# Optimization experiments

Measured on AMD Instinct MI355X. Metric: run time of the kernel, lower is better.

The kernel has to match this reference:

```python
import jax, jax.numpy as jnp
from jax import lax
import numpy as np

B, L, DIM = 4, 4096, 512
H, HD = 8, 64            # num_heads, head_dim
CHUNK = 128              # chunk size for chunk-recurrent lightning attention
LN_EPS = 1e-5


def _slopes(h):
    # _build_slope_tensor for power-of-2 heads: 2^(-8*(i+1)/h), cast through fp16
    s = np.array([2.0 ** (-8.0 * (i + 1) / h) for i in range(h)], dtype=np.float32)
    return jnp.asarray(s.astype(np.float16).astype(np.float32))  # [h]


def _layernorm(x, w, b):
    mu = jnp.mean(x, axis=-1, keepdims=True)
    var = jnp.mean((x - mu) ** 2, axis=-1, keepdims=True)
    return (x - mu) * lax.rsqrt(var + LN_EPS) * w + b


def _rmsnorm(x, gamma):
    # F.normalize(x, dim=-1) * sqrt(d) * gamma ; gamma [h,1,d] broadcasts over [b,h,l,d]
    n = x / jnp.maximum(jnp.linalg.norm(x, axis=-1, keepdims=True), 1e-12)
    return n * (HD ** 0.5) * gamma


def _lightning_attn(q, k, v, slopes):
    # q,k,v: [b,h,L,d]; causal linear attention with per-head decay exp(-s*(t-j))
    b, h, l, d = q.shape
    nc = l // CHUNK
    s = slopes[:, None, None]                      # [h,1,1]
    r = jnp.arange(CHUNK, dtype=q.dtype)
    diff = r[:, None] - r[None, :]                 # [C,C]
    Dintra = jnp.where(diff >= 0, jnp.exp(-s * diff), 0.0)   # [h,C,C]
    q_dec = jnp.exp(-slopes[:, None] * r[None, :])           # [h,C] decay from chunk start
    k_dec = jnp.exp(-slopes[:, None] * (CHUNK - r[None, :])) # [h,C] decay to next chunk start
    c_dec = jnp.exp(-slopes * CHUNK)                         # [h]

    def to_chunks(t):
        return t.reshape(b, h, nc, CHUNK, d).transpose(2, 0, 1, 3, 4)  # [nc,b,h,C,d]

    qc, kc, vc = to_chunks(q), to_chunks(k), to_chunks(v)

    def step(kv, inp):
        qi, ki, vi = inp                                       # [b,h,C,d]
        scores = jnp.einsum('bhid,bhjd->bhij', qi, ki) * Dintra[None]
        intra = jnp.einsum('bhij,bhjd->bhid', scores, vi)
        inter = jnp.einsum('bhcd,bhde->bhce', qi * q_dec[None, :, :, None], kv)
        kv = kv * c_dec[None, :, None, None] + jnp.einsum(
            'bhcd,bhce->bhde', ki * k_dec[None, :, :, None], vi)
        return kv, intra + inter

    kv0 = jnp.zeros((b, h, d, d), q.dtype)
    _, out = lax.scan(step, kv0, (qc, kc, vc))                 # [nc,b,h,C,d]
    return out.transpose(1, 2, 0, 3, 4).reshape(b, h, l, d)


def setup_inputs() -> dict:
    key = jax.random.key(0)
    ks = jax.random.split(key, 8)
    std = lambda fan_in: 1.0 / np.sqrt(fan_in)
    return {
        'x': jax.random.normal(ks[0], (B, L, DIM), jnp.float32),
        'ln1_w': jnp.ones((DIM,), jnp.float32),
        'ln1_b': jnp.zeros((DIM,), jnp.float32),
        'rel_bias': 0.02 * jax.random.normal(ks[1], (1, L, DIM), jnp.float32),
        'qkv_w': std(DIM) * jax.random.normal(ks[2], (3 * DIM, DIM), jnp.float32),
        'qkv_b': jnp.zeros((3 * DIM,), jnp.float32),
        'gq': jnp.ones((H, 1, HD), jnp.float32) / (HD ** 0.5),
        'gk': jnp.ones((H, 1, HD), jnp.float32) / (HD ** 0.5),
        'proj_w': std(DIM) * jax.random.normal(ks[3], (DIM, DIM), jnp.float32),
        'proj_b': jnp.zeros((DIM,), jnp.float32),
        'ln2_w': jnp.ones((DIM,), jnp.float32),
        'ln2_b': jnp.zeros((DIM,), jnp.float32),
        'fc1_w': std(DIM) * jax.random.normal(ks[4], (4 * DIM, DIM), jnp.float32),
        'fc1_b': jnp.zeros((4 * DIM,), jnp.float32),
        'fc2_w': std(4 * DIM) * jax.random.normal(ks[5], (DIM, 4 * DIM), jnp.float32),
        'fc2_b': jnp.zeros((DIM,), jnp.float32),
    }


def reference(x, ln1_w, ln1_b, rel_bias, qkv_w, qkv_b, gq, gk,
              proj_w, proj_b, ln2_w, ln2_b, fc1_w, fc1_b, fc2_w, fc2_b):
    slopes = _slopes(H)
    b, l, c = x.shape
    shortcut = x
    h = _layernorm(x, ln1_w, ln1_b)
    # --- LightningAttention ---
    h = h + rel_bias
    qkv = (h @ qkv_w.T + qkv_b).reshape(b, l, 3, H, HD).transpose(2, 0, 3, 1, 4)
    q, k, v = qkv[0], qkv[1], qkv[2]                     # [b,h,l,d]
    q = _rmsnorm(q * (HD ** -0.5), gq)
    k = _rmsnorm(k, gk)
    o = _lightning_attn(q, k, v, slopes)                 # [b,h,l,d]
    o = o.reshape(b, l, c)                               # faithful to source: reshape, no head transpose
    o = o @ proj_w.T + proj_b
    x = o + shortcut
    # --- MLP ---
    shortcut = x
    h = _layernorm(x, ln2_w, ln2_b)
    h = jax.nn.gelu(h @ fc1_w.T + fc1_b, approximate=False)
    h = h @ fc2_w.T + fc2_b
    return h + shortcut
```

## Files before the change

### kernel.cpp

```cpp
#include <hip/hip_runtime.h>
#include <math.h>

typedef unsigned short u16;
typedef __bf16 bf16x8 __attribute__((ext_vector_type(8)));
typedef float f32x4 __attribute__((ext_vector_type(4)));

#define DEVI static __device__ __forceinline__

DEVI float b2f(u16 u) { union { unsigned int i; float f; } w; w.i = ((unsigned int)u) << 16; return w.f; }
DEVI u16 f2b(float f) {
  union { float f; unsigned int i; } w; w.f = f;
  unsigned int r = (w.i + 0x7FFFu + ((w.i >> 16) & 1u)) >> 16;
  return (u16)r;
}
DEVI u16 cvt_bf16(float f) { __bf16 h = (__bf16)f; union { __bf16 h; u16 u; } w; w.h = h; return w.u; }

DEVI float fast_gelu(float v) {
  float x2 = v * v;
  float p = fmaf(0.10294357f, x2, 2.30215855f);
  float ex = exp2f(-v * p);
  return v * __builtin_amdgcn_rcpf(1.0f + ex);
}

__global__ void conv4_kernel(const float* __restrict__ s0, u16* __restrict__ d0, int n0,
                             const float* __restrict__ s1, u16* __restrict__ d1, int n1,
                             const float* __restrict__ s2, u16* __restrict__ d2, int n2,
                             const float* __restrict__ s3, u16* __restrict__ d3, int n3) {
  int i = blockIdx.x * 256 + threadIdx.x;
  int st = gridDim.x * 256;
  int tot = n0 + n1 + n2 + n3;
  for (; i < tot; i += st) {
    int j = i;
    if (j < n0) { d0[j] = f2b(s0[j]); continue; }
    j -= n0;
    if (j < n1) { d1[j] = f2b(s1[j]); continue; }
    j -= n1;
    if (j < n2) { d2[j] = f2b(s2[j]); continue; }
    j -= n2;
    d3[j] = f2b(s3[j]);
  }
}

template<int ADD_REL>
__global__ __launch_bounds__(256) void ln_kernel(
    const float* __restrict__ x, const float* __restrict__ w, const float* __restrict__ bb,
    const float* __restrict__ rel, u16* __restrict__ out) {
  int row = blockIdx.x;
  int t = threadIdx.x;
  const float* xr = x + (size_t)row * 512;
  float v0 = xr[t], v1 = xr[t + 256];
  float s = v0 + v1, ss = v0 * v0 + v1 * v1;
#pragma unroll
  for (int o = 32; o > 0; o >>= 1) { s += __shfl_down(s, o); ss += __shfl_down(ss, o); }
  __shared__ float rs[4], rss[4];
  int lane = t & 63, wid = t >> 6;
  if (lane == 0) { rs[wid] = s; rss[wid] = ss; }
  __syncthreads();
  s = rs[0] + rs[1] + rs[2] + rs[3];
  ss = rss[0] + rss[1] + rss[2] + rss[3];
  float mu = s * (1.0f / 512.0f);
  float inv = rsqrtf(ss * (1.0f / 512.0f) - mu * mu + 1e-5f);
  float o0 = (v0 - mu) * inv * w[t] + bb[t];
  float o1 = (v1 - mu) * inv * w[t + 256] + bb[t + 256];
  if (ADD_REL) {
    const float* rr = rel + (size_t)(row & 4095) * 512;
    o0 += rr[t]; o1 += rr[t + 256];
  }
  u16* orow = out + (size_t)row * 512;
  orow[t] = f2b(o0);
  orow[t + 256] = f2b(o1);
}

template<int EPI, int TM, int NSLOT>
__global__ __launch_bounds__(256) void gemm_bt_kernel(
    const u16* __restrict__ A, const u16* __restrict__ W,
    const float* __restrict__ bias, int M, int N, int K, int NBN,
    const float* __restrict__ resid, u16* __restrict__ outb,
    u16* __restrict__ q_out, u16* __restrict__ k_out, u16* __restrict__ v_out,
    float* __restrict__ outf, const float* __restrict__ gq, const float* __restrict__ gk) {
  constexpr int WM   = TM / 2;
  constexpr int NI   = TM / 32;
  constexpr int CA   = TM / 64;
  constexpr int SLOT = (TM + 128) * 32;
  __shared__ __align__(16) u16 sbuf[NSLOT * SLOT];
  int nwg = gridDim.x, wg = blockIdx.x;
  int wgs = (wg & 7) * (nwg >> 3) + (wg >> 3);
  int bn = wgs % NBN, bm = wgs / NBN;
  int m0 = bm * TM, n0 = bn * 128;
  int t = threadIdx.x, lane = t & 63, wid = t >> 6;
  int wrM = (wid >> 1) * WM, wc = (wid & 1) * 64;
  int fr = lane & 15, fk = (lane >> 4) * 8;
  int srowA = wid * (TM / 4) + (lane >> 2);
  int srowB = wid * 32 + (lane >> 2);
  int scol = (lane & 3) * 8;
  const u16* gA = A + (size_t)(m0 + srowA) * K + scol;
  const u16* gB = W + (size_t)(n0 + srowB) * K + scol;
  f32x4 acc[NI][4] = {};
  auto AS = [&](int sel) { return &sbuf[sel * SLOT]; };
  auto BS = [&](int sel) { return &sbuf[sel * SLOT + TM * 32]; };
  auto STAGE = [&](int sel, int k0) {
    u16* lA = AS(sel) + wid * (CA * 512);
    u16* lB = BS(sel) + wid * 1024;
#pragma unroll
    for (int c = 0; c < CA; ++c)
      __builtin_amdgcn_global_load_lds(gA + k0 + c * 16 * K, lA + c * 512, 16, 0, 0);
    __builtin_amdgcn_global_load_lds(gB + k0,          lB,       16, 0, 0);
    __builtin_amdgcn_global_load_lds(gB + k0 + 16 * K, lB + 512, 16, 0, 0);
  };
  auto COMPUTE = [&](int sel) {
    bf16x8 af[NI], bfr[4];
#pragma unroll
    for (int i = 0; i < NI; ++i) af[i] = *(const bf16x8*)&AS(sel)[(wrM + i * 16 + fr) * 32 + fk];
#pragma unroll
    for (int j = 0; j < 4; ++j) bfr[j] = *(const bf16x8*)&BS(sel)[(wc + j * 16 + fr) * 32 + fk];
#pragma unroll
    for (int i = 0; i < NI; ++i)
#pragma unroll
      for (int j = 0; j < 4; ++j)
        acc[i][j] = __builtin_amdgcn_mfma_f32_16x16x32_bf16(af[i], bfr[j], acc[i][j], 0, 0, 0);
  };
  if constexpr (NSLOT == 2) {
    STAGE(0, 0);
    asm volatile("s_waitcnt vmcnt(0)" ::: "memory");
    __builtin_amdgcn_s_barrier();
    int cur = 0;
    for (int k0 = 0; k0 < K; k0 += 32) {
      if (k0 + 32 < K) STAGE(cur ^ 1, k0 + 32);
      COMPUTE(cur);
      asm volatile("s_waitcnt vmcnt(0)" ::: "memory");
      __builtin_amdgcn_s_barrier();
      cur ^= 1;
    }
  } else {
    STAGE(0, 0);
    STAGE(1, 32);
    int cur = 0, nxt = 2;
    for (int k0 = 0; k0 < K; k0 += 32) {
      if (k0 + 32 < K) {
        if constexpr (CA == 4) { asm volatile("s_waitcnt vmcnt(6)" ::: "memory"); }
        else                   { asm volatile("s_waitcnt vmcnt(4)" ::: "memory"); }
      } else {
        asm volatile("s_waitcnt vmcnt(0)" ::: "memory");
      }
      __builtin_amdgcn_s_barrier();
      if (k0 + 64 < K) {
        STAGE(nxt, k0 + 64);
        nxt = (nxt == 2) ? 0 : nxt + 1;
      }
      COMPUTE(cur);
      cur = (cur == 2) ? 0 : cur + 1;
    }
  }
  __syncthreads();
  int fq = lane >> 4;
  constexpr int LP = 68;
  float* lbuf = (float*)sbuf + wid * 2048;
  float bv[4];
#pragma unroll
  for (int j = 0; j < 4; ++j) bv[j] = bias[n0 + wc + j * 16 + fr];
  int rr = lane >> 2, c0 = (lane & 3) * 16;
  int nb = n0 + wc;
  int which = nb >> 9, head = (nb >> 6) & 7;
  float ggv[16];
  if (EPI == 0 && which != 2) {
    const float* gg = (which == 0) ? gq : gk;
#pragma unroll
    for (int e = 0; e < 16; ++e) ggv[e] = gg[head * 64 + c0 + e];
  }
#pragma unroll
  for (int i = 0; i < NI; ++i) {
#pragma unroll
    for (int j = 0; j < 4; ++j)
#pragma unroll
      for (int jj = 0; jj < 4; ++jj)
        lbuf[(fq * 4 + jj) * LP + j * 16 + fr] = acc[i][j][jj] + bv[j];
    float v[16];
#pragma unroll
    for (int g = 0; g < 4; ++g) {
      f32x4 r4 = *(const f32x4*)&lbuf[rr * LP + c0 + g * 4];
#pragma unroll
      for (int e = 0; e < 4; ++e) v[g * 4 + e] = r4[e];
    }
    int gm = m0 + wrM + i * 16 + rr;
    if (EPI == 0) {
      u16* dst = (which == 0) ? q_out : (which == 1) ? k_out : v_out;
      int b = gm >> 12, l = gm & 4095;
      size_t rowbase = (((size_t)(b * 8 + head) * 4096) + l) * 64 + c0;
      union { u16 h[16]; uint4 q[2]; } pk;
      if (which == 2) {
#pragma unroll
        for (int e = 0; e < 16; ++e) pk.h[e] = cvt_bf16(v[e]);
      } else {
        float ssum = 0.f;
#pragma unroll
        for (int e = 0; e < 16; ++e) ssum += v[e] * v[e];
        ssum += __shfl_xor(ssum, 1);
        ssum += __shfl_xor(ssum, 2);
        float inv = 8.0f / fmaxf(sqrtf(ssum), 1e-12f);
#pragma unroll
        for (int e = 0; e < 16; ++e) pk.h[e] = cvt_bf16(v[e] * inv * ggv[e]);
      }
      *(uint4*)&dst[rowbase] = pk.q[0];
      *(uint4*)&dst[rowbase + 8] = pk.q[1];
    } else if (EPI == 1) {
      size_t idx = (size_t)gm * 512 + n0 + wc + c0;
#pragma unroll
      for (int g = 0; g < 4; ++g) {
        f32x4 r = *(const f32x4*)&resid[idx + g * 4];
        f32x4 o;
#pragma unroll
        for (int e = 0; e < 4; ++e) o[e] = v[g * 4 + e] + r[e];
        *(f32x4*)&outf[idx + g * 4] = o;
      }
    } else {
      union { u16 h[16]; uint4 q[2]; } pk;
#pragma unroll
      for (int e = 0; e < 16; ++e) pk.h[e] = cvt_bf16(fast_gelu(v[e]));
      size_t idx = (size_t)gm * (size_t)N + n0 + wc + c0;
      *(uint4*)&outb[idx] = pk.q[0];
      *(uint4*)&outb[idx + 8] = pk.q[1];
    }
  }
}

__global__ __launch_bounds__(256) void attn_kv_kernel(
    const u16* __restrict__ k, const u16* __restrict__ v, float* __restrict__ P) {
  constexpr int LT = 136;
  __shared__ __align__(16) u16 kT_s[64 * LT];
  __shared__ __align__(16) u16 vT_s[64 * LT];
  __shared__ float kdec[128];
  int bid = blockIdx.x;
  int bh = bid >> 5;
  float sl = exp2f(-(float)((bh & 7) + 1));
  int t = threadIdx.x, lane = t & 63, wid = t >> 6;
  for (int i = t; i < 128; i += 256) kdec[i] = expf(-sl * (float)(128 - i));
  const u16* kb = k + (size_t)bid * 8192;
  const u16* vb = v + (size_t)bid * 8192;
  __syncthreads();
  int fr = lane & 15, fk = (lane >> 4) * 8, fq = lane >> 4;
#pragma unroll
  for (int i = 0; i < 16; ++i) {
    int seg = t + i * 256;
    int j = seg >> 5, dd = (seg & 31) * 2;
    unsigned int kp = *(const unsigned int*)&kb[(size_t)j * 64 + dd];
    float kd = kdec[j];
    kT_s[dd * LT + j] = f2b(b2f((u16)(kp & 0xFFFFu)) * kd);
    kT_s[(dd + 1) * LT + j] = f2b(b2f((u16)(kp >> 16)) * kd);
    unsigned int vp = *(const unsigned int*)&vb[(size_t)j * 64 + dd];
    vT_s[dd * LT + j] = (u16)(vp & 0xFFFFu);
    vT_s[(dd + 1) * LT + j] = (u16)(vp >> 16);
  }
  __syncthreads();
  f32x4 accKV[4] = {};
#pragma unroll
  for (int kk = 0; kk < 4; ++kk) {
    bf16x8 akt = *(const bf16x8*)&kT_s[(wid * 16 + fr) * LT + kk * 32 + fk];
#pragma unroll
    for (int j = 0; j < 4; ++j) {
      bf16x8 bvt = *(const bf16x8*)&vT_s[(j * 16 + fr) * LT + kk * 32 + fk];
      accKV[j] = __builtin_amdgcn_mfma_f32_16x16x32_bf16(akt, bvt, accKV[j], 0, 0, 0);
    }
  }
  float* PT = (float*)kT_s;
  __syncthreads();
#pragma unroll
  for (int j = 0; j < 4; ++j)
#pragma unroll
    for (int jj = 0; jj < 4; ++jj) {
      int dd = wid * 16 + fq * 4 + jj;
      int e = j * 16 + fr;
      PT[e * 68 + dd] = accKV[j][jj];
    }
  __syncthreads();
  float* Pg = P + (size_t)bid * 4096;
  int e = t >> 2, d0 = (t & 3) * 16;
#pragma unroll
  for (int g = 0; g < 4; ++g) {
    f32x4 val = *(const f32x4*)&PT[e * 68 + d0 + g * 4];
    *(f32x4*)&Pg[(size_t)e * 64 + d0 + g * 4] = val;
  }
}

__global__ __launch_bounds__(256) void attn_scan_kernel(
    const float* __restrict__ P, u16* __restrict__ kvst) {
  int bh = blockIdx.x, t = threadIdx.x;
  float sl = exp2f(-(float)((bh & 7) + 1));
  float cdec = expf(-sl * 128.0f);
  float kv[16];
#pragma unroll
  for (int i = 0; i < 16; ++i) kv[i] = 0.f;
  for (int c = 0; c < 32; ++c) {
    size_t off = (((size_t)bh * 32 + c) * 4096) + (size_t)t * 16;
    union { u16 st[16]; uint4 v4[4]; } u;
#pragma unroll
    for (int i = 0; i < 16; ++i) u.st[i] = f2b(kv[i]);
    *(uint4*)&kvst[off] = u.v4[0];
    *(uint4*)&kvst[off + 8] = u.v4[1];
#pragma unroll
    for (int g = 0; g < 4; ++g) {
      f32x4 p = *(const f32x4*)&P[off + g * 4];
#pragma unroll
      for (int e = 0; e < 4; ++e) kv[g * 4 + e] = cdec * kv[g * 4 + e] + p[e];
    }
  }
}

__global__ __launch_bounds__(256) void attn_out_kernel(
    const u16* __restrict__ q, const u16* __restrict__ k, const u16* __restrict__ v,
    const u16* __restrict__ kvst, u16* __restrict__ o) {
  constexpr int LQ = 72, LT = 136, LS = 136, LKV = 72;
  __shared__ __align__(16) u16 sm[31744];
  u16* q_s  = sm;
  u16* k_s  = sm + 9216;
  u16* vT_s = sm + 18432;
  u16* kvT_s = sm + 27136;
  u16* S_s  = sm;
  __shared__ float rowf[128], colf[128];
  int bid = blockIdx.x;
  int bh = bid >> 5;
  float sl = exp2f(-(float)((bh & 7) + 1));
  int t = threadIdx.x, lane = t & 63, wid = t >> 6;
  for (int i = t; i < 128; i += 256) {
    rowf[i] = expf(-sl * i);
    colf[i] = expf(sl * i);
  }
  const u16* qb = q + (size_t)bid * 8192;
  const u16* kb = k + (size_t)bid * 8192;
  const u16* vb = v + (size_t)bid * 8192;
  const u16* kvb = kvst + (size_t)bid * 4096;
  u16* ob = o + (size_t)bid * 8192;
  int fr = lane & 15, fk = (lane >> 4) * 8, fq = lane >> 4;
#pragma unroll
  for (int i = 0; i < 4; ++i) {
    int seg = t + i * 256;
    int r = seg >> 3, cc = (seg & 7) * 8;
    *(uint4*)&q_s[r * LQ + cc] = *(const uint4*)&qb[(size_t)r * 64 + cc];
    *(uint4*)&k_s[r * LQ + cc] = *(const uint4*)&kb[(size_t)r * 64 + cc];
  }
#pragma unroll
  for (int i = 0; i < 16; ++i) {
    int seg = t + i * 256;
    int j = seg >> 5, dd = (seg & 31) * 2;
    unsigned int vp = *(const unsigned int*)&vb[(size_t)j * 64 + dd];
    vT_s[dd * LT + j] = (u16)(vp & 0xFFFFu);
    vT_s[(dd + 1) * LT + j] = (u16)(vp >> 16);
  }
#pragma unroll
  for (int i = 0; i < 2; ++i) {
    int seg = t + i * 256;
    int e = seg >> 3, dd = (seg & 7) * 8;
    *(uint4*)&kvT_s[e * LKV + dd] = *(const uint4*)&kvb[(size_t)e * 64 + dd];
  }
  __syncthreads();
  f32x4 accS[2][8] = {};
  f32x4 accI[2][4] = {};
#pragma unroll
  for (int kk = 0; kk < 2; ++kk) {
    bf16x8 aq0 = *(const bf16x8*)&q_s[(wid * 32 + fr) * LQ + kk * 32 + fk];
    bf16x8 aq1 = *(const bf16x8*)&q_s[(wid * 32 + 16 + fr) * LQ + kk * 32 + fk];
#pragma unroll
    for (int j = 0; j < 8; ++j) {
      bf16x8 bk = *(const bf16x8*)&k_s[(j * 16 + fr) * LQ + kk * 32 + fk];
      accS[0][j] = __builtin_amdgcn_mfma_f32_16x16x32_bf16(aq0, bk, accS[0][j], 0, 0, 0);
      accS[1][j] = __builtin_amdgcn_mfma_f32_16x16x32_bf16(aq1, bk, accS[1][j], 0, 0, 0);
    }
#pragma unroll
    for (int j = 0; j < 4; ++j) {
      bf16x8 bkv = *(const bf16x8*)&kvT_s[(j * 16 + fr) * LKV + kk * 32 + fk];
      accI[0][j] = __builtin_amdgcn_mfma_f32_16x16x32_bf16(aq0, bkv, accI[0][j], 0, 0, 0);
      accI[1][j] = __builtin_amdgcn_mfma_f32_16x16x32_bf16(aq1, bkv, accI[1][j], 0, 0, 0);
    }
  }
  __syncthreads();
#pragma unroll
  for (int i = 0; i < 2; ++i)
#pragma unroll
    for (int j = 0; j < 8; ++j)
#pragma unroll
      for (int jj = 0; jj < 4; ++jj) {
        int si = wid * 32 + i * 16 + fq * 4 + jj;
        int sj = j * 16 + fr;
        float val = (si >= sj) ? accS[i][j][jj] * rowf[si] * colf[sj] : 0.0f;
        S_s[si * LS + sj] = f2b(val);
      }
  __syncthreads();
  f32x4 accO[2][4] = {};
#pragma unroll
  for (int kk = 0; kk < 4; ++kk) {
    bf16x8 as0 = *(const bf16x8*)&S_s[(wid * 32 + fr) * LS + kk * 32 + fk];
    bf16x8 as1 = *(const bf16x8*)&S_s[(wid * 32 + 16 + fr) * LS + kk * 32 + fk];
#pragma unroll
    for (int j = 0; j < 4; ++j) {
      bf16x8 bvt = *(const bf16x8*)&vT_s[(j * 16 + fr) * LT + kk * 32 + fk];
      accO[0][j] = __builtin_amdgcn_mfma_f32_16x16x32_bf16(as0, bvt, accO[0][j], 0, 0, 0);
      accO[1][j] = __builtin_amdgcn_mfma_f32_16x16x32_bf16(as1, bvt, accO[1][j], 0, 0, 0);
    }
  }
#pragma unroll
  for (int i = 0; i < 2; ++i)
#pragma unroll
    for (int j = 0; j < 4; ++j)
#pragma unroll
      for (int jj = 0; jj < 4; ++jj) {
        int li = wid * 32 + i * 16 + fq * 4 + jj;
        int e = j * 16 + fr;
        float val = accO[i][j][jj] + rowf[li] * accI[i][j][jj];
        ob[(size_t)li * 64 + e] = f2b(val);
      }
}

extern "C" void kernel_launch(void* const* d_in, const int* in_sizes, int n_in,
                              void* d_out, int out_size, void* d_ws, size_t ws_size,
                              hipStream_t stream) {
  const float* x      = (const float*)d_in[0];
  const float* ln1_w  = (const float*)d_in[1];
  const float* ln1_b  = (const float*)d_in[2];
  const float* rel    = (const float*)d_in[3];
  const float* qkv_w  = (const float*)d_in[4];
  const float* qkv_b  = (const float*)d_in[5];
  const float* gq     = (const float*)d_in[6];
  const float* gk     = (const float*)d_in[7];
  const float* proj_w = (const float*)d_in[8];
  const float* proj_b = (const float*)d_in[9];
  const float* ln2_w  = (const float*)d_in[10];
  const float* ln2_b  = (const float*)d_in[11];
  const float* fc1_w  = (const float*)d_in[12];
  const float* fc1_b  = (const float*)d_in[13];
  const float* fc2_w  = (const float*)d_in[14];
  const float* fc2_b  = (const float*)d_in[15];

  char* ws = (char*)d_ws;
  size_t off = 0;
  auto alloc = [&](size_t bytes) { char* p = ws + off; off += (bytes + 255) & ~(size_t)255; return p; };
  u16* w_qkv  = (u16*)alloc((size_t)1536 * 512 * 2);
  u16* w_proj = (u16*)alloc((size_t)512 * 512 * 2);
  u16* w_fc1  = (u16*)alloc((size_t)2048 * 512 * 2);
  u16* w_fc2  = (u16*)alloc((size_t)512 * 2048 * 2);
  u16* h_buf  = (u16*)alloc((size_t)16384 * 512 * 2);
  u16* q_buf  = (u16*)alloc((size_t)8388608 * 2);
  u16* k_buf  = (u16*)alloc((size_t)8388608 * 2);
  u16* v_buf  = (u16*)alloc((size_t)8388608 * 2);
  u16* o_buf  = (u16*)alloc((size_t)8388608 * 2);
  float* x2   = (float*)alloc((size_t)8388608 * 4);
  u16* mid    = q_buf;
  float* P_glob  = x2;
  u16*   kv_state = (u16*)(x2 + 4194304);

  conv4_kernel<<<1024, 256, 0, stream>>>(qkv_w, w_qkv, 1536 * 512,
                                         proj_w, w_proj, 512 * 512,
                                         fc1_w, w_fc1, 2048 * 512,
                                         fc2_w, w_fc2, 512 * 2048);

  ln_kernel<1><<<16384, 256, 0, stream>>>(x, ln1_w, ln1_b, rel, h_buf);

  gemm_bt_kernel<0, 128, 3><<<1536, 256, 0, stream>>>(h_buf, w_qkv, qkv_b, 16384, 1536, 512, 12,
      nullptr, nullptr, q_buf, k_buf, v_buf,
      nullptr, gq, gk);

  attn_kv_kernel<<<1024, 256, 0, stream>>>(k_buf, v_buf, P_glob);
  attn_scan_kernel<<<32, 256, 0, stream>>>(P_glob, kv_state);
  attn_out_kernel<<<1024, 256, 0, stream>>>(q_buf, k_buf, v_buf, kv_state, o_buf);

  gemm_bt_kernel<1, 128, 3><<<512, 256, 0, stream>>>(o_buf, w_proj, proj_b, 16384, 512, 512, 4,
      x, nullptr, nullptr, nullptr, nullptr, x2, nullptr, nullptr);

  ln_kernel<0><<<16384, 256, 0, stream>>>(x2, ln2_w, ln2_b, nullptr, h_buf);

  gemm_bt_kernel<2, 128, 3><<<2048, 256, 0, stream>>>(h_buf, w_fc1, fc1_b, 16384, 2048, 512, 16,
      nullptr, mid, nullptr, nullptr, nullptr, nullptr, nullptr, nullptr);

  gemm_bt_kernel<1, 128, 3><<<512, 256, 0, stream>>>(mid, w_fc2, fc2_b, 16384, 512, 2048, 4,
      x2, nullptr, nullptr, nullptr, nullptr, (float*)d_out, nullptr, nullptr);

  (void)in_sizes; (void)n_in; (void)out_size; (void)ws_size;
}
```

Before: 265.9 us.

## Add 256x256-tile 8-wave GEMM with interleaved LDS prefetch for FC1+GELU

Replaces the FC1 GEMM (previously 128x128 tiles, 256 threads) with a dedicated kernel using 256x256 tiles, 8 waves, and direct global-to-LDS loads. The next K-tile's A/B stages are issued in pieces between MFMA sub-blocks to overlap memory with compute. Larger tiles raise arithmetic intensity and cut redundant operand loads, but use 128KB of LDS and many accumulators, which limits occupancy. The workgroup index is also remapped for L2 locality.

After: 265.8 us. Within noise of the previous version (-0.0%).

```diff
diff --git a/kernel.cpp b/kernel.cpp
--- a/kernel.cpp
+++ b/kernel.cpp
@@ -223,6 +223,146 @@
   }
 }
 
+__global__ __launch_bounds__(512, 2) void gemm8_gelu_kernel(
+    const u16* __restrict__ A, const u16* __restrict__ W,
+    const float* __restrict__ bias, int M, int N, int K, int NBN,
+    u16* __restrict__ outb) {
+  __shared__ __align__(16) u16 sbuf[65536];
+  int nwg = gridDim.x, wg = blockIdx.x;
+  int wgs = (wg & 7) * (nwg >> 3) + (wg >> 3);
+  int bn = wgs % NBN, bm = wgs / NBN;
+  int m0 = bm * 256, n0 = bn * 256;
+  int t = threadIdx.x, lane = t & 63, wid = t >> 6;
+  int wm = wid >> 2, wn = wid & 3;
+  int fr = lane & 15, fk = (lane >> 4) * 8, fq = lane >> 4;
+  int srow = t >> 3, scol = (t & 7) * 8;
+  const u16* gA = A + (size_t)(m0 + srow) * K + scol;
+  const u16* gB = W + (size_t)(n0 + srow) * K + scol;
+  auto STAGE_A = [&](int db, int R0, int kt) {
+    u16* lds = &sbuf[db * 16384 + R0 * 64 + wid * 512];
+    const u16* g = gA + (size_t)R0 * K + kt * 64;
+    __builtin_amdgcn_global_load_lds(g,                    lds,        16, 0, 0);
+    __builtin_amdgcn_global_load_lds(g + (size_t)64 * K,   lds + 4096, 16, 0, 0);
+  };
+  auto STAGE_B = [&](int db, int R0, int kt) {
+    u16* lds = &sbuf[32768 + db * 16384 + R0 * 64 + wid * 512];
+    const u16* g = gB + (size_t)R0 * K + kt * 64;
+    __builtin_amdgcn_global_load_lds(g,                    lds,        16, 0, 0);
+    __builtin_amdgcn_global_load_lds(g + (size_t)64 * K,   lds + 4096, 16, 0, 0);
+  };
+  f32x4 acc[8][4] = {};
+  int NT = K >> 6;
+  STAGE_A(0, 0, 0); STAGE_A(0, 128, 0); STAGE_B(0, 0, 0); STAGE_B(0, 128, 0);
+  asm volatile("s_waitcnt vmcnt(0)" ::: "memory");
+  __builtin_amdgcn_s_barrier();
+  for (int kt = 0; kt < NT; ++kt) {
+    int db = kt & 1, dbn = db ^ 1;
+    const u16* Ab = &sbuf[db * 16384];
+    const u16* Bb = &sbuf[32768 + db * 16384];
+    bf16x8 bfr[4][2];
+    bool pre = (kt + 1 < NT);
+    if (pre) STAGE_A(dbn, 0, kt + 1);
+#pragma unroll
+    for (int nj = 0; nj < 4; ++nj)
+#pragma unroll
+      for (int kh = 0; kh < 2; ++kh)
+        bfr[nj][kh] = *(const bf16x8*)&Bb[(wn * 64 + nj * 16 + fr) * 64 + kh * 32 + fk];
+    {
+      bf16x8 af[2][2];
+#pragma unroll
+      for (int m = 0; m < 2; ++m)
+#pragma unroll
+        for (int kh = 0; kh < 2; ++kh)
+          af[m][kh] = *(const bf16x8*)&Ab[(wm * 128 + (0 + m) * 16 + fr) * 64 + kh * 32 + fk];
+#pragma unroll
+      for (int m = 0; m < 2; ++m)
+#pragma unroll
+        for (int nj = 0; nj < 4; ++nj)
+#pragma unroll
+          for (int kh = 0; kh < 2; ++kh)
+            acc[0 + m][nj] = __builtin_amdgcn_mfma_f32_16x16x32_bf16(af[m][kh], bfr[nj][kh], acc[0 + m][nj], 0, 0, 0);
+    }
+    if (pre) STAGE_A(dbn, 128, kt + 1);
+    {
+      bf16x8 af[2][2];
+#pragma unroll
+      for (int m = 0; m < 2; ++m)
+#pragma unroll
+        for (int kh = 0; kh < 2; ++kh)
+          af[m][kh] = *(const bf16x8*)&Ab[(wm * 128 + (2 + m) * 16 + fr) * 64 + kh * 32 + fk];
+#pragma unroll
+      for (int m = 0; m < 2; ++m)
+#pragma unroll
+        for (int nj = 0; nj < 4; ++nj)
+#pragma unroll
+          for (int kh = 0; kh < 2; ++kh)
+            acc[2 + m][nj] = __builtin_amdgcn_mfma_f32_16x16x32_bf16(af[m][kh], bfr[nj][kh], acc[2 + m][nj], 0, 0, 0);
+    }
+    if (pre) STAGE_B(dbn, 0, kt + 1);
+    {
+      bf16x8 af[2][2];
+#pragma unroll
+      for (int m = 0; m < 2; ++m)
+#pragma unroll
+        for (int kh = 0; kh < 2; ++kh)
+          af[m][kh] = *(const bf16x8*)&Ab[(wm * 128 + (4 + m) * 16 + fr) * 64 + kh * 32 + fk];
+#pragma unroll
+      for (int m = 0; m < 2; ++m)
+#pragma unroll
+        for (int nj = 0; nj < 4; ++nj)
+#pragma unroll
+          for (int kh = 0; kh < 2; ++kh)
+            acc[4 + m][nj] = __builtin_amdgcn_mfma_f32_16x16x32_bf16(af[m][kh], bfr[nj][kh], acc[4 + m][nj], 0, 0, 0);
+    }
+    if (pre) STAGE_B(dbn, 128, kt + 1);
+    {
+      bf16x8 af[2][2];
+#pragma unroll
+      for (int m = 0; m < 2; ++m)
+#pragma unroll
+        for (int kh = 0; kh < 2; ++kh)
+          af[m][kh] = *(const bf16x8*)&Ab[(wm * 128 + (6 + m) * 16 + fr) * 64 + kh * 32 + fk];
+#pragma unroll
+      for (int m = 0; m < 2; ++m)
+#pragma unroll
+        for (int nj = 0; nj < 4; ++nj)
+#pragma unroll
+          for (int kh = 0; kh < 2; ++kh)
+            acc[6 + m][nj] = __builtin_amdgcn_mfma_f32_16x16x32_bf16(af[m][kh], bfr[nj][kh], acc[6 + m][nj], 0, 0, 0);
+    }
+    asm volatile("s_waitcnt vmcnt(0)" ::: "memory");
+    __builtin_amdgcn_s_barrier();
+  }
+  constexpr int LP = 68;
+  float* lbuf = (float*)sbuf + wid * 2048;
+  float bv[4];
+#pragma unroll
+  for (int j = 0; j < 4; ++j) bv[j] = bias[n0 + wn * 64 + j * 16 + fr];
+  int rr = lane >> 2, c0 = (lane & 3) * 16;
+#pragma unroll
+  for (int i = 0; i < 8; ++i) {
+#pragma unroll
+    for (int j = 0; j < 4; ++j)
+#pragma unroll
+      for (int jj = 0; jj < 4; ++jj)
+        lbuf[(fq * 4 + jj) * LP + j * 16 + fr] = acc[i][j][jj] + bv[j];
+    float v[16];
+#pragma unroll
+    for (int g = 0; g < 4; ++g) {
+      f32x4 r4 = *(const f32x4*)&lbuf[rr * LP + c0 + g * 4];
+#pragma unroll
+      for (int e = 0; e < 4; ++e) v[g * 4 + e] = r4[e];
+    }
+    int gm = m0 + wm * 128 + i * 16 + rr;
+    union { u16 h[16]; uint4 q[2]; } pk;
+#pragma unroll
+    for (int e = 0; e < 16; ++e) pk.h[e] = cvt_bf16(fast_gelu(v[e]));
+    size_t idx = (size_t)gm * (size_t)N + n0 + wn * 64 + c0;
+    *(uint4*)&outb[idx] = pk.q[0];
+    *(uint4*)&outb[idx + 8] = pk.q[1];
+  }
+}
+
 __global__ __launch_bounds__(256) void attn_kv_kernel(
     const u16* __restrict__ k, const u16* __restrict__ v, float* __restrict__ P) {
   constexpr int LT = 136;
@@ -466,8 +606,8 @@
 
   ln_kernel<0><<<16384, 256, 0, stream>>>(x2, ln2_w, ln2_b, nullptr, h_buf);
 
-  gemm_bt_kernel<2, 128, 3><<<2048, 256, 0, stream>>>(h_buf, w_fc1, fc1_b, 16384, 2048, 512, 16,
-      nullptr, mid, nullptr, nullptr, nullptr, nullptr, nullptr, nullptr);
+  gemm8_gelu_kernel<<<512, 512, 0, stream>>>(h_buf, w_fc1, fc1_b, 16384, 2048, 512, 8,
+      mid);
 
   gemm_bt_kernel<1, 128, 3><<<512, 256, 0, stream>>>(mid, w_fc2, fc2_b, 16384, 512, 2048, 4,
       x2, nullptr, nullptr, nullptr, nullptr, (float*)d_out, nullptr, nullptr);
```
